# Kernel optimization log

Measured on AMD Instinct MI355X. Metric: run time of the kernel, lower is better.

## Reference

```python
import jax, jax.numpy as jnp
import numpy as np

DIM = 16            # Hilbert space dimension
D = DIM * DIM       # superoperator / vectorized-density dimension (256)
N_TS = 128          # number of timesteps
N_CTRLS = 2         # number of control fields
DT = 0.02           # timestep
SQUARINGS = 6       # scaling-and-squaring steps for matrix_exp
TAYLOR_TERMS = 12   # Taylor (Horner) order for matrix_exp


def setup_inputs() -> dict:
    key = jax.random.key(0)
    ks = jax.random.split(key, 12)
    s = 0.05  # keep generator norms small so expm(A*dt) is well-conditioned
    D2 = (D, D)
    ctrls_real = jax.random.normal(ks[0], (N_TS, N_CTRLS), jnp.float32)
    ctrls_im = jax.random.normal(ks[1], (N_TS, N_CTRLS), jnp.float32)
    dyn_gen_re = s * jax.random.normal(ks[2], D2, jnp.float32)
    dyn_gen_im = s * jax.random.normal(ks[3], D2, jnp.float32)
    ctrl_gen_re = s * jax.random.normal(ks[4], (N_CTRLS, 2, D, D), jnp.float32)
    ctrl_gen_im = s * jax.random.normal(ks[5], (N_CTRLS, 2, D, D), jnp.float32)
    # initial / target: vectorized density-like states (identity/DIM + noise)
    eye_vec = (jnp.eye(DIM, dtype=jnp.float32) / DIM).reshape(D)
    initial_re = eye_vec + 0.01 * jax.random.normal(ks[6], (D,), jnp.float32)
    initial_im = 0.01 * jax.random.normal(ks[7], (D,), jnp.float32)
    target_re = eye_vec + 0.01 * jax.random.normal(ks[8], (D,), jnp.float32)
    target_im = 0.01 * jax.random.normal(ks[9], (D,), jnp.float32)
    return dict(ctrls_real=ctrls_real, ctrls_im=ctrls_im,
                dyn_gen_re=dyn_gen_re, dyn_gen_im=dyn_gen_im,
                ctrl_gen_re=ctrl_gen_re, ctrl_gen_im=ctrl_gen_im,
                initial_re=initial_re, initial_im=initial_im,
                target_re=target_re, target_im=target_im)


def _expm(A):
    """Differentiable matrix exponential: scaling-and-squaring + Taylor (Horner)."""
    A = A / (2.0 ** SQUARINGS)
    I = jnp.eye(A.shape[-1], dtype=A.dtype)
    R = I
    for k in range(TAYLOR_TERMS, 0, -1):
        R = I + (A @ R) / k
    for _ in range(SQUARINGS):
        R = R @ R
    return R


def _evolve(cr, ci, dyn, Gr, Gi, s0):
    # control generators: _get_ctrl_gen -> cr*(G0+G1) + 1j*ci*(G0-G1)
    G0 = Gr[:, 0] + 1j * Gi[:, 0]   # [n_ctrls, D, D]
    G1 = Gr[:, 1] + 1j * Gi[:, 1]
    Gp = G0 + G1
    Gm = G0 - G1
    crc = cr.astype(Gp.dtype)
    cic = ci.astype(Gm.dtype)
    # per-timestep dynamics generator A_k = dyn + sum_j ctrl terms  [n_ts, D, D]
    A = (dyn[None, :, :]
         + jnp.einsum('kj,jab->kab', crc, Gp)
         + 1j * jnp.einsum('kj,jab->kab', cic, Gm))
    props = jax.vmap(_expm)(A * DT)  # [n_ts, D, D]
    diag_idx = jnp.arange(DIM) * (DIM + 1)  # trace indices of vec(rho)

    def step(s, P):
        s = P @ s
        s = s / s[diag_idx].sum()  # trace normalization
        return s, None

    sT, _ = jax.lax.scan(step, s0, props)
    return sT


def reference(ctrls_real, ctrls_im, dyn_gen_re, dyn_gen_im,
              ctrl_gen_re, ctrl_gen_im, initial_re, initial_im,
              target_re, target_im):
    dyn = dyn_gen_re + 1j * dyn_gen_im
    s0 = initial_re + 1j * initial_im
    sT = _evolve(ctrls_real, ctrls_im, dyn, ctrl_gen_re, ctrl_gen_im, s0)
    tgt = target_re + 1j * target_im
    fid_err = jnp.linalg.norm((sT - tgt).reshape(DIM, DIM))  # Frobenius norm
    return sT, fid_err
```

## Files before the change

kernel.cpp:

```cpp
#include <hip/hip_runtime.h>
#include <math.h>

#define DD    256
#define PLQ   65536
#define SLOTB 131072
#define NTS   128
#define DT_C  0.02f

typedef unsigned short u16;
typedef unsigned int   u32;
typedef __attribute__((ext_vector_type(8))) short s16x8;
typedef __attribute__((ext_vector_type(4))) float f32x4;

typedef __attribute__((address_space(1))) const unsigned int GU32;
typedef __attribute__((address_space(3))) unsigned int LU32;

__device__ __forceinline__ u32 swzB(u32 b) {
    return b ^ (((((b >> 7) ^ (b >> 10)) & 7u)) << 4);
}
__device__ __forceinline__ u16 f2bf(float f) {
    u32 u = __float_as_uint(f);
    return (u16)((u + 0x7FFFu + ((u >> 16) & 1u)) >> 16);
}
__device__ __forceinline__ float bf2f(u16 h) {
    return __uint_as_float(((u32)h) << 16);
}
__device__ __forceinline__ void gll16(const u16* g, char* ldsBase, u32 ldsByteOff) {
    u32 off = (u32)__builtin_amdgcn_readfirstlane((int)ldsByteOff);
    __builtin_amdgcn_global_load_lds((GU32*)g, (LU32*)(ldsBase + off), 16, 0, 0);
}

__global__ __launch_bounds__(256)
void build_kernel(const float* __restrict__ cr, const float* __restrict__ ci,
                  const float* __restrict__ dre, const float* __restrict__ dimg,
                  const float* __restrict__ gre, const float* __restrict__ gim,
                  u16* __restrict__ Xn, int ts0)
{
    const int ts = blockIdx.y;
    const int k  = ts0 + ts;
    const int i4 = (blockIdx.x * 256 + threadIdx.x) * 4;

    const float c0f = cr[2*k], c1f = cr[2*k+1];
    const float e0f = ci[2*k], e1f = ci[2*k+1];

    const float4 g0r = *(const float4*)&gre[0*PLQ + i4];
    const float4 g1r = *(const float4*)&gre[1*PLQ + i4];
    const float4 g2r = *(const float4*)&gre[2*PLQ + i4];
    const float4 g3r = *(const float4*)&gre[3*PLQ + i4];
    const float4 g0i = *(const float4*)&gim[0*PLQ + i4];
    const float4 g1i = *(const float4*)&gim[1*PLQ + i4];
    const float4 g2i = *(const float4*)&gim[2*PLQ + i4];
    const float4 g3i = *(const float4*)&gim[3*PLQ + i4];
    const float4 d_r = *(const float4*)&dre[i4];
    const float4 d_i = *(const float4*)&dimg[i4];
    const float* gr00 = &g0r.x; const float* gr01 = &g1r.x;
    const float* gr10 = &g2r.x; const float* gr11 = &g3r.x;
    const float* gi00 = &g0i.x; const float* gi01 = &g1i.x;
    const float* gi10 = &g2i.x; const float* gi11 = &g3i.x;
    const float* dr4  = &d_r.x; const float* di4  = &d_i.x;

    ushort4 hr, hi;
    u16* hrp = &hr.x; u16* hip = &hi.x;
    #pragma unroll
    for (int j = 0; j < 4; ++j) {
        const float are = dr4[j] + c0f*(gr00[j]+gr01[j]) + c1f*(gr10[j]+gr11[j])
                                 - e0f*(gi00[j]-gi01[j]) - e1f*(gi10[j]-gi11[j]);
        const float aim = di4[j] + c0f*(gi00[j]+gi01[j]) + c1f*(gi10[j]+gi11[j])
                                 + e0f*(gr00[j]-gr01[j]) + e1f*(gr10[j]-gr11[j]);
        hrp[j] = f2bf(DT_C * are);
        hip[j] = f2bf(DT_C * aim);
    }
    u16* X = Xn + (size_t)ts * SLOTB;
    *(ushort4*)&X[i4]       = hr;
    *(ushort4*)&X[PLQ + i4] = hi;
}

__global__ __launch_bounds__(256, 8)
void cgemm64(const u16* __restrict__ Ab, const u16* __restrict__ Bb,
             u16* __restrict__ outN,
             const u16* __restrict__ X1b, const u16* __restrict__ X2b,
             float aN, float bN1, float bN2,
             int aS, int aO, int bS, int bO, int cS, int cO,
             int x1S, int x1O, int x2S, int x2O)
{
    __shared__ char lds[32768];

    const u32 nwg = 16u * (u32)gridDim.z;
    const u32 wg  = (u32)blockIdx.x + 4u*(u32)blockIdx.y + 16u*(u32)blockIdx.z;
    const u32 q   = nwg >> 3;
    const u32 w   = (wg & 7u) * q + (wg >> 3);
    const int bn = (int)(w & 3u) * 64;
    const int bm = (int)((w >> 2) & 3u) * 64;
    const int z  = (int)(w >> 4);

    const u16* __restrict__ A = Ab + (size_t)(z*aS + aO) * SLOTB;
    const u16* __restrict__ B = Bb + (size_t)(z*bS + bO) * SLOTB;

    const int t = threadIdx.x;

    const u32 b0 = (u32)t * 16u, b1 = 4096u + (u32)t * 16u;
    const u32 L0 = swzB(b0),     L1 = swzB(b1);
    const int rA0 = (int)(L0 >> 7), kA0 = (int)((L0 & 127u) >> 1);
    const int rA1 = (int)(L1 >> 7), kA1 = (int)((L1 & 127u) >> 1);
    const u32 wvoff = ((u32)(t >> 6)) * 1024u;

    const u16* pA0 = A + (size_t)(bm + rA0)*DD + kA0;
    const u16* pA1 = A + (size_t)(bm + rA1)*DD + kA1;

    const int kRow = t >> 3;
    const int nCh  = t & 7;

    const int wv = t >> 6, ln = t & 63;
    const int wrow = (wv >> 1) * 32, wcol = (wv & 1) * 32;
    const int lg = ln >> 4, lc = ln & 15;

    f32x4 accR[2][2], accI[2][2];
    #pragma unroll
    for (int i = 0; i < 2; ++i)
        #pragma unroll
        for (int j = 0; j < 2; ++j) {
            accR[i][j] = (f32x4){0.f,0.f,0.f,0.f};
            accI[i][j] = (f32x4){0.f,0.f,0.f,0.f};
        }

    {
        gll16(pA0,       lds, wvoff +     0u);
        gll16(pA1,       lds, wvoff +  4096u);
        gll16(pA0 + PLQ, lds, wvoff +  8192u);
        gll16(pA1 + PLQ, lds, wvoff + 12288u);
        #pragma unroll
        for (int h = 0; h < 2; ++h) {
            const int kk = h*32 + kRow;
            const s16x8 vr = *(const s16x8*)(B +       (size_t)kk*DD + bn + nCh*8);
            const s16x8 vi = *(const s16x8*)(B + PLQ + (size_t)kk*DD + bn + nCh*8);
            #pragma unroll
            for (int e = 0; e < 8; ++e) {
                const u32 off = swzB((u32)(nCh*8 + e)*128u + (u32)kk*2u);
                *(u16*)(lds + 16384 + off) = (u16)vr[e];
                *(u16*)(lds + 24576 + off) = (u16)vi[e];
            }
        }
    }
    __syncthreads();

    for (int it = 0; it < 4; ++it) {
        s16x8 nvr0, nvi0, nvr1, nvi1;
        if (it < 3) {
            const int k1 = 64*(it + 1);
            nvr0 = *(const s16x8*)(B +       (size_t)(k1 + kRow)*DD + bn + nCh*8);
            nvi0 = *(const s16x8*)(B + PLQ + (size_t)(k1 + kRow)*DD + bn + nCh*8);
            nvr1 = *(const s16x8*)(B +       (size_t)(k1 + 32 + kRow)*DD + bn + nCh*8);
            nvi1 = *(const s16x8*)(B + PLQ + (size_t)(k1 + 32 + kRow)*DD + bn + nCh*8);
        }

        #pragma unroll
        for (int s = 0; s < 2; ++s) {
            s16x8 ar[2], ai[2], br[2], bi[2];
            #pragma unroll
            for (int fm = 0; fm < 2; ++fm) {
                const u32 so = swzB((u32)(wrow + fm*16 + lc)*128u + (u32)(s*4 + lg)*16u);
                ar[fm] = *(const s16x8*)(lds + so);
                ai[fm] = *(const s16x8*)(lds + 8192 + so);
            }
            #pragma unroll
            for (int fn = 0; fn < 2; ++fn) {
                const u32 so = swzB((u32)(wcol + fn*16 + lc)*128u + (u32)(s*4 + lg)*16u);
                br[fn] = *(const s16x8*)(lds + 16384 + so);
                bi[fn] = *(const s16x8*)(lds + 24576 + so);
            }
            #pragma unroll
            for (int fm = 0; fm < 2; ++fm)
                #pragma unroll
                for (int fn = 0; fn < 2; ++fn) {
                    accI[fm][fn] = __builtin_amdgcn_mfma_f32_16x16x32_bf16(ar[fm], bi[fn], accI[fm][fn], 0, 0, 0);
                    accI[fm][fn] = __builtin_amdgcn_mfma_f32_16x16x32_bf16(ai[fm], br[fn], accI[fm][fn], 0, 0, 0);
                }
            #pragma unroll
            for (int fm = 0; fm < 2; ++fm) ai[fm] ^= (short)0x8000u;
            #pragma unroll
            for (int fm = 0; fm < 2; ++fm)
                #pragma unroll
                for (int fn = 0; fn < 2; ++fn) {
                    accR[fm][fn] = __builtin_amdgcn_mfma_f32_16x16x32_bf16(ar[fm], br[fn], accR[fm][fn], 0, 0, 0);
                    accR[fm][fn] = __builtin_amdgcn_mfma_f32_16x16x32_bf16(ai[fm], bi[fn], accR[fm][fn], 0, 0, 0);
                }
        }

        if (it < 3) {
            const int k1 = 64*(it + 1);
            __syncthreads();
            gll16(pA0 + k1,       lds, wvoff +     0u);
            gll16(pA1 + k1,       lds, wvoff +  4096u);
            gll16(pA0 + PLQ + k1, lds, wvoff +  8192u);
            gll16(pA1 + PLQ + k1, lds, wvoff + 12288u);
            #pragma unroll
            for (int e = 0; e < 8; ++e) {
                const u32 off0 = swzB((u32)(nCh*8 + e)*128u + (u32)kRow*2u);
                const u32 off1 = swzB((u32)(nCh*8 + e)*128u + (u32)(32 + kRow)*2u);
                *(u16*)(lds + 16384 + off0) = (u16)nvr0[e];
                *(u16*)(lds + 24576 + off0) = (u16)nvi0[e];
                *(u16*)(lds + 16384 + off1) = (u16)nvr1[e];
                *(u16*)(lds + 24576 + off1) = (u16)nvi1[e];
            }
            __syncthreads();
        }
    }

    __syncthreads();
    #pragma unroll
    for (int fm = 0; fm < 2; ++fm)
        #pragma unroll
        for (int fn = 0; fn < 2; ++fn) {
            const int rb = wrow + fm*16 + lg*4;
            const int c  = wcol + fn*16 + lc;
            #pragma unroll
            for (int j = 0; j < 4; ++j) {
                const u32 ob = swzB((u32)(rb + j)*128u + (u32)c*2u);
                *(u16*)(lds +        ob) = f2bf(aN * accR[fm][fn][j]);
                *(u16*)(lds + 8192 + ob) = f2bf(aN * accI[fm][fn][j]);
            }
        }
    __syncthreads();

    u16* oN = outN + (size_t)(z*cS + cO) * SLOTB;
    const u16* x1 = X1b ? X1b + (size_t)(z*x1S + x1O) * SLOTB : nullptr;
    const u16* x2 = X2b ? X2b + (size_t)(z*x2S + x2O) * SLOTB : nullptr;

    const int orow = t >> 2;
    const u32 och  = ((u32)t & 3u) * 32u;
    const size_t gOff = (size_t)(bm + orow)*DD + bn + (och >> 1);

    #pragma unroll
    for (int pl = 0; pl < 2; ++pl) {
        const u32 lb   = (u32)pl * 8192u + (u32)orow * 128u + och;
        const size_t g = gOff + (size_t)pl * PLQ;
        #pragma unroll
        for (int h = 0; h < 2; ++h) {
            const s16x8 cv = *(const s16x8*)(lds + swzB(lb + (u32)h*16u));
            float o[8];
            #pragma unroll
            for (int e = 0; e < 8; ++e) o[e] = bf2f((u16)cv[e]);
            if (x1) {
                const s16x8 xv = *(const s16x8*)(x1 + g + h*8);
                #pragma unroll
                for (int e = 0; e < 8; ++e) o[e] += bN1 * bf2f((u16)xv[e]);
            }
            if (x2) {
                const s16x8 xv = *(const s16x8*)(x2 + g + h*8);
                #pragma unroll
                for (int e = 0; e < 8; ++e) o[e] += bN2 * bf2f((u16)xv[e]);
            }
            s16x8 ov;
            #pragma unroll
            for (int e = 0; e < 8; ++e) ov[e] = (short)f2bf(o[e]);
            *(s16x8*)(oN + g + h*8) = ov;
        }
    }
}

__global__ __launch_bounds__(256)
void final_kernel(const u16* __restrict__ Et,
                  const float* __restrict__ s0r, const float* __restrict__ s0i,
                  const float* __restrict__ tgr, const float* __restrict__ tgi,
                  float* __restrict__ out, int outSize)
{
    __shared__ float sr[DD], si[DD], red[DD];
    __shared__ float cR, cI;
    const int t = threadIdx.x;
    sr[t] = s0r[t];
    si[t] = s0i[t];
    __syncthreads();

    const u16* Er = Et + (size_t)t*DD;
    const u16* Ei = Er + PLQ;
    float ar = sr[t], ai = si[t];
    for (int kk = 0; kk < DD/8; ++kk) {
        const s16x8 er = *(const s16x8*)(Er + kk*8);
        const s16x8 ei = *(const s16x8*)(Ei + kk*8);
        #pragma unroll
        for (int jj = 0; jj < 8; ++jj) {
            const float pr = bf2f((u16)er[jj]);
            const float pi = bf2f((u16)ei[jj]);
            const int k = kk*8 + jj;
            ar += pr*sr[k] - pi*si[k];
            ai += pr*si[k] + pi*sr[k];
        }
    }
    __syncthreads();
    sr[t] = ar; si[t] = ai;
    __syncthreads();

    if (t == 0) {
        float xr = 0.f, xi = 0.f;
        for (int i = 0; i < 16; ++i) { xr += sr[i*17]; xi += si[i*17]; }
        cR = xr; cI = xi;
    }
    __syncthreads();

    const float den = cR*cR + cI*cI;
    const float str = (ar*cR + ai*cI) / den;
    const float sti = (ai*cR - ar*cI) / den;

    const float dr = str - tgr[t];
    const float di = sti - tgi[t];
    red[t] = dr*dr + di*di;
    __syncthreads();
    for (int s = 128; s > 0; s >>= 1) {
        if (t < s) red[t] += red[t + s];
        __syncthreads();
    }
    const float fid = sqrtf(red[0]);

    if (outSize >= 2*DD + 1) {
        out[2*t] = str; out[2*t+1] = sti;
        if (t == 0) out[2*DD] = fid;
    } else if (outSize == 2*DD) {
        out[2*t] = str; out[2*t+1] = sti;
    } else {
        out[t] = str;
        if (t == 0 && outSize > DD) out[DD] = fid;
    }
}

extern "C" void kernel_launch(void* const* d_in, const int* in_sizes, int n_in,
                              void* d_out, int out_size, void* d_ws, size_t ws_size,
                              hipStream_t stream)
{
    (void)in_sizes; (void)n_in;
    const float* cr   = (const float*)d_in[0];
    const float* ci   = (const float*)d_in[1];
    const float* dre  = (const float*)d_in[2];
    const float* dimg = (const float*)d_in[3];
    const float* gre  = (const float*)d_in[4];
    const float* gim  = (const float*)d_in[5];
    const float* s0r  = (const float*)d_in[6];
    const float* s0i  = (const float*)d_in[7];
    const float* tgr  = (const float*)d_in[8];
    const float* tgi  = (const float*)d_in[9];

    const float c2 = 0.5f, c3i = 1.f/6.f;

    u16* ws = (u16*)d_ws;
    const long slots = (long)(ws_size / 2) / SLOTB;

    if (slots >= 384) {
        u16* RX = ws;
        u16* R1 = ws + 128L * SLOTB;
        u16* R2 = ws + 256L * SLOTB;

        build_kernel<<<dim3(PLQ/1024, 128), 256, 0, stream>>>(
            cr, ci, dre, dimg, gre, gim, RX, 0);

        const dim3 g128(4, 4, 128);
        cgemm64<<<g128, 256, 0, stream>>>(RX, RX, R1, nullptr, nullptr,
            1.f, 0.f, 0.f,
            1,0, 1,0, 1,0, 0,0, 0,0);
        cgemm64<<<g128, 256, 0, stream>>>(R1, RX, R2, RX, R1,
            c3i, 1.f, c2,
            1,0, 1,0, 1,0, 1,0, 1,0);

        u16* cur = R2;
        u16* oth = R1;
        for (int n = 128; n > 1; n >>= 1) {
            cgemm64<<<dim3(4, 4, n/2), 256, 0, stream>>>(
                cur, cur, oth, cur, cur,
                1.f, 1.f, 1.f,
                2,1, 2,0, 1,0, 2,1, 2,0);
            u16* tmp = cur; cur = oth; oth = tmp;
        }
        final_kernel<<<1, 256, 0, stream>>>(cur, s0r, s0i, tgr, tgi,
                                            (float*)d_out, out_size);
    } else {
        u16* P  = ws;
        u16* CB = ws + 128L * SLOTB;
        int C = (int)((slots - 128) / 2);
        if (C > NTS) C = NTS;
        if (C < 32)  C = 32;

        for (int ts0 = 0; ts0 < NTS; ts0 += C) {
            int nb = NTS - ts0; if (nb > C) nb = C;
            u16* Xn = CB;
            u16* P2 = CB + 1L*C*SLOTB;

            build_kernel<<<dim3(PLQ/1024, nb), 256, 0, stream>>>(
                cr, ci, dre, dimg, gre, gim, Xn, ts0);

            const dim3 grid(4, 4, nb);
            cgemm64<<<grid, 256, 0, stream>>>(Xn, Xn, P2, nullptr, nullptr,
                1.f, 0.f, 0.f,
                1,0, 1,0, 1,0, 0,0, 0,0);
            cgemm64<<<grid, 256, 0, stream>>>(P2, Xn, P, Xn, P2,
                c3i, 1.f, c2,
                1,0, 1,0, 1,ts0, 1,0, 1,0);
        }

        u16* cur = P;
        u16* oth = CB;
        for (int n = 128; n > 1; n >>= 1) {
            cgemm64<<<dim3(4, 4, n/2), 256, 0, stream>>>(
                cur, cur, oth, cur, cur,
                1.f, 1.f, 1.f,
                2,1, 2,0, 1,0, 2,1, 2,0);
            u16* tmp = cur; cur = oth; oth = tmp;
        }
        final_kernel<<<1, 256, 0, stream>>>(cur, s0r, s0i, tgr, tgi,
                                            (float*)d_out, out_size);
    }
}
```

Baseline: 174.4 us.

## Double-buffer cgemm64 LDS with K=32 stages and async prefetch

Restructures the complex bf16 GEMM main loop from four K=64 stages into eight K=32 stages that ping-pong between two LDS buffers. The next stage's A tile is prefetched by direct global-to-LDS loads and its B tile into registers while MFMAs run on the current buffer. Waits use explicit vmcnt/lgkmcnt and raw s_barrier, and MFMA sections run at raised wave priority. The launch-bounds occupancy hint drops from 8 to 6 waves. This aims to hide global-load latency and cut synchronisation stalls, but it doubles the number of barriers per tile and relies on hand-written waitcnt ordering being correct.

Result: slower. 182.8 us (+4.8%).

```diff
diff --git a/kernel.cpp b/kernel.cpp
--- a/kernel.cpp
+++ b/kernel.cpp
@@ -17,6 +17,9 @@
 
 __device__ __forceinline__ u32 swzB(u32 b) {
     return b ^ (((((b >> 7) ^ (b >> 10)) & 7u)) << 4);
+}
+__device__ __forceinline__ u32 swz32(u32 b) {
+    return b ^ (((b >> 7) & 7u) << 4);
 }
 __device__ __forceinline__ u16 f2bf(float f) {
     u32 u = __float_as_uint(f);
@@ -75,7 +78,7 @@
     *(ushort4*)&X[PLQ + i4] = hi;
 }
 
-__global__ __launch_bounds__(256, 8)
+__global__ __launch_bounds__(256, 6)
 void cgemm64(const u16* __restrict__ Ab, const u16* __restrict__ Bb,
              u16* __restrict__ outN,
              const u16* __restrict__ X1b, const u16* __restrict__ X2b,
@@ -98,14 +101,12 @@
 
     const int t = threadIdx.x;
 
-    const u32 b0 = (u32)t * 16u, b1 = 4096u + (u32)t * 16u;
-    const u32 L0 = swzB(b0),     L1 = swzB(b1);
-    const int rA0 = (int)(L0 >> 7), kA0 = (int)((L0 & 127u) >> 1);
-    const int rA1 = (int)(L1 >> 7), kA1 = (int)((L1 & 127u) >> 1);
+    const u32 b0 = (u32)t * 16u;
+    const u32 L0 = swz32(b0);
+    const int rA0 = (int)(L0 >> 6), kA0 = (int)((L0 & 63u) >> 1);
     const u32 wvoff = ((u32)(t >> 6)) * 1024u;
 
     const u16* pA0 = A + (size_t)(bm + rA0)*DD + kA0;
-    const u16* pA1 = A + (size_t)(bm + rA1)*DD + kA1;
 
     const int kRow = t >> 3;
     const int nCh  = t & 7;
@@ -123,90 +124,75 @@
             accI[i][j] = (f32x4){0.f,0.f,0.f,0.f};
         }
 
+    s16x8 vr, vi;
     {
-        gll16(pA0,       lds, wvoff +     0u);
-        gll16(pA1,       lds, wvoff +  4096u);
-        gll16(pA0 + PLQ, lds, wvoff +  8192u);
-        gll16(pA1 + PLQ, lds, wvoff + 12288u);
-        #pragma unroll
-        for (int h = 0; h < 2; ++h) {
-            const int kk = h*32 + kRow;
-            const s16x8 vr = *(const s16x8*)(B +       (size_t)kk*DD + bn + nCh*8);
-            const s16x8 vi = *(const s16x8*)(B + PLQ + (size_t)kk*DD + bn + nCh*8);
-            #pragma unroll
-            for (int e = 0; e < 8; ++e) {
-                const u32 off = swzB((u32)(nCh*8 + e)*128u + (u32)kk*2u);
-                *(u16*)(lds + 16384 + off) = (u16)vr[e];
-                *(u16*)(lds + 24576 + off) = (u16)vi[e];
-            }
-        }
-    }
-    __syncthreads();
-
-    for (int it = 0; it < 4; ++it) {
-        s16x8 nvr0, nvi0, nvr1, nvi1;
-        if (it < 3) {
-            const int k1 = 64*(it + 1);
-            nvr0 = *(const s16x8*)(B +       (size_t)(k1 + kRow)*DD + bn + nCh*8);
-            nvi0 = *(const s16x8*)(B + PLQ + (size_t)(k1 + kRow)*DD + bn + nCh*8);
-            nvr1 = *(const s16x8*)(B +       (size_t)(k1 + 32 + kRow)*DD + bn + nCh*8);
-            nvi1 = *(const s16x8*)(B + PLQ + (size_t)(k1 + 32 + kRow)*DD + bn + nCh*8);
-        }
-
-        #pragma unroll
-        for (int s = 0; s < 2; ++s) {
-            s16x8 ar[2], ai[2], br[2], bi[2];
-            #pragma unroll
-            for (int fm = 0; fm < 2; ++fm) {
-                const u32 so = swzB((u32)(wrow + fm*16 + lc)*128u + (u32)(s*4 + lg)*16u);
-                ar[fm] = *(const s16x8*)(lds + so);
-                ai[fm] = *(const s16x8*)(lds + 8192 + so);
-            }
+        gll16(pA0,       lds, wvoff +    0u);
+        gll16(pA0 + PLQ, lds, wvoff + 4096u);
+        vr = *(const s16x8*)(B +       (size_t)kRow*DD + bn + nCh*8);
+        vi = *(const s16x8*)(B + PLQ + (size_t)kRow*DD + bn + nCh*8);
+    }
+
+    for (int it = 0; it < 8; ++it) {
+        const u32 cb = (u32)(it & 1) * 16384u;
+        const u32 sb = cb ^ 16384u;
+        s16x8 nr, ni;
+        if (it < 7) {
+            const int k1 = 32*(it + 1);
+            gll16(pA0 + k1,       lds, sb + wvoff +    0u);
+            gll16(pA0 + PLQ + k1, lds, sb + wvoff + 4096u);
+            nr = *(const s16x8*)(B +       (size_t)(k1 + kRow)*DD + bn + nCh*8);
+            ni = *(const s16x8*)(B + PLQ + (size_t)(k1 + kRow)*DD + bn + nCh*8);
+            asm volatile("s_waitcnt vmcnt(4)" ::: "memory");
+        } else {
+            asm volatile("s_waitcnt vmcnt(0)" ::: "memory");
+        }
+        __builtin_amdgcn_sched_barrier(0);
+
+        #pragma unroll
+        for (int e = 0; e < 8; ++e) {
+            const u32 off = swz32((u32)(nCh*8 + e)*64u + (u32)kRow*2u);
+            *(u16*)(lds + cb +  8192 + off) = (u16)vr[e];
+            *(u16*)(lds + cb + 12288 + off) = (u16)vi[e];
+        }
+        asm volatile("s_waitcnt lgkmcnt(0)\n\ts_barrier" ::: "memory");
+
+        __builtin_amdgcn_s_setprio(1);
+        s16x8 ar[2], ai[2], br[2], bi[2];
+        #pragma unroll
+        for (int fm = 0; fm < 2; ++fm) {
+            const u32 so = swz32((u32)(wrow + fm*16 + lc)*64u + (u32)lg*16u);
+            ar[fm] = *(const s16x8*)(lds + cb + so);
+            ai[fm] = *(const s16x8*)(lds + cb + 4096 + so);
+        }
+        #pragma unroll
+        for (int fn = 0; fn < 2; ++fn) {
+            const u32 so = swz32((u32)(wcol + fn*16 + lc)*64u + (u32)lg*16u);
+            br[fn] = *(const s16x8*)(lds + cb +  8192 + so);
+            bi[fn] = *(const s16x8*)(lds + cb + 12288 + so);
+        }
+        #pragma unroll
+        for (int fm = 0; fm < 2; ++fm)
             #pragma unroll
             for (int fn = 0; fn < 2; ++fn) {
-                const u32 so = swzB((u32)(wcol + fn*16 + lc)*128u + (u32)(s*4 + lg)*16u);
-                br[fn] = *(const s16x8*)(lds + 16384 + so);
-                bi[fn] = *(const s16x8*)(lds + 24576 + so);
-            }
-            #pragma unroll
-            for (int fm = 0; fm < 2; ++fm)
-                #pragma unroll
-                for (int fn = 0; fn < 2; ++fn) {
-                    accI[fm][fn] = __builtin_amdgcn_mfma_f32_16x16x32_bf16(ar[fm], bi[fn], accI[fm][fn], 0, 0, 0);
-                    accI[fm][fn] = __builtin_amdgcn_mfma_f32_16x16x32_bf16(ai[fm], br[fn], accI[fm][fn], 0, 0, 0);
-                }
-            #pragma unroll
-            for (int fm = 0; fm < 2; ++fm) ai[fm] ^= (short)0x8000u;
-            #pragma unroll
-            for (int fm = 0; fm < 2; ++fm)
-                #pragma unroll
-                for (int fn = 0; fn < 2; ++fn) {
-                    accR[fm][fn] = __builtin_amdgcn_mfma_f32_16x16x32_bf16(ar[fm], br[fn], accR[fm][fn], 0, 0, 0);
-                    accR[fm][fn] = __builtin_amdgcn_mfma_f32_16x16x32_bf16(ai[fm], bi[fn], accR[fm][fn], 0, 0, 0);
-                }
-        }
-
-        if (it < 3) {
-            const int k1 = 64*(it + 1);
-            __syncthreads();
-            gll16(pA0 + k1,       lds, wvoff +     0u);
-            gll16(pA1 + k1,       lds, wvoff +  4096u);
-            gll16(pA0 + PLQ + k1, lds, wvoff +  8192u);
-            gll16(pA1 + PLQ + k1, lds, wvoff + 12288u);
-            #pragma unroll
-            for (int e = 0; e < 8; ++e) {
-                const u32 off0 = swzB((u32)(nCh*8 + e)*128u + (u32)kRow*2u);
-                const u32 off1 = swzB((u32)(nCh*8 + e)*128u + (u32)(32 + kRow)*2u);
-                *(u16*)(lds + 16384 + off0) = (u16)nvr0[e];
-                *(u16*)(lds + 24576 + off0) = (u16)nvi0[e];
-                *(u16*)(lds + 16384 + off1) = (u16)nvr1[e];
-                *(u16*)(lds + 24576 + off1) = (u16)nvi1[e];
-            }
-            __syncthreads();
-        }
-    }
-
-    __syncthreads();
+                accI[fm][fn] = __builtin_amdgcn_mfma_f32_16x16x32_bf16(ar[fm], bi[fn], accI[fm][fn], 0, 0, 0);
+                accI[fm][fn] = __builtin_amdgcn_mfma_f32_16x16x32_bf16(ai[fm], br[fn], accI[fm][fn], 0, 0, 0);
+            }
+        #pragma unroll
+        for (int fm = 0; fm < 2; ++fm) ai[fm] ^= (short)0x8000u;
+        #pragma unroll
+        for (int fm = 0; fm < 2; ++fm)
+            #pragma unroll
+            for (int fn = 0; fn < 2; ++fn) {
+                accR[fm][fn] = __builtin_amdgcn_mfma_f32_16x16x32_bf16(ar[fm], br[fn], accR[fm][fn], 0, 0, 0);
+                accR[fm][fn] = __builtin_amdgcn_mfma_f32_16x16x32_bf16(ai[fm], bi[fn], accR[fm][fn], 0, 0, 0);
+            }
+        __builtin_amdgcn_s_setprio(0);
+
+        asm volatile("s_barrier" ::: "memory");
+        vr = nr; vi = ni;
+    }
+
+    asm volatile("s_barrier" ::: "memory");
     #pragma unroll
     for (int fm = 0; fm < 2; ++fm)
         #pragma unroll
```
